# Kernel optimization log

Measured on AMD Instinct MI355X. Metric: run time of the kernel, lower is better.

The kernel has to match this reference:

```python
import jax, jax.numpy as jnp
import numpy as np

N_PAIRS = 64000
N_ATOMS = 16000
N_PAIR_FEATURES = 8
N_HIDDEN = 100


def setup_inputs() -> dict:
    key = jax.random.key(0)
    k1, k2, k3, k4 = jax.random.split(key, 4)
    pair_features = jax.random.normal(k1, (N_PAIRS, N_PAIR_FEATURES), dtype=jnp.float32)
    atom_features = jax.random.normal(k2, (N_ATOMS, N_HIDDEN), dtype=jnp.float32)
    atom_to_pair = jax.random.randint(k3, (N_PAIRS, 2), 0, N_ATOMS, dtype=jnp.int32)
    W = jax.random.normal(k4, (N_PAIR_FEATURES, N_HIDDEN * N_HIDDEN), dtype=jnp.float32) * 0.1
    b = jnp.zeros((N_HIDDEN * N_HIDDEN,), dtype=jnp.float32)
    return {"pair_features": pair_features, "atom_features": atom_features,
            "atom_to_pair": atom_to_pair, "W": W, "b": b}


def reference(pair_features, atom_features, atom_to_pair, W, b):
    n_atoms, n_hidden = atom_features.shape
    # Dense projection: [E, F] @ [F, H*H] -> per-edge HxH matrices
    A = (pair_features @ W + b).reshape(-1, n_hidden, n_hidden)  # [E, H, H]
    # Gather source-atom features (column 1 of atom_to_pair)
    src = atom_features[atom_to_pair[:, 1]]                      # [E, H]
    # Batched matrix-vector multiply per edge
    msg = jnp.einsum('eij,ej->ei', A, src)                       # [E, H]
    # Scatter-reduce messages onto destination atoms (column 0)
    return jax.ops.segment_sum(msg, atom_to_pair[:, 0], num_segments=n_atoms)
```

## Files before the change

kernel.cpp:

```cpp
#include <hip/hip_runtime.h>
#include <hip/hip_bf16.h>

#define N_PAIRS   64000
#define N_ATOMS   16000
#define N_FEAT    8
#define N_HIDDEN  100
#define SW        1024
#define SKL       936
#define MAX_DEG   64

#define SETUP_BLOCKS (112 * 1024 / 256)
#define HIST_BLOCKS  (N_PAIRS / 256)

typedef __attribute__((ext_vector_type(8))) short bf16x8_t;
typedef __attribute__((ext_vector_type(4))) float f32x4_t;

__global__ __launch_bounds__(256) void setup_hist(const float* __restrict__ W,
                                                  const float* __restrict__ b,
                                                  const int* __restrict__ a2p,
                                                  const float* __restrict__ pf,
                                                  __hip_bfloat16* __restrict__ wtb2,
                                                  int* __restrict__ deg,
                                                  unsigned* __restrict__ bucket,
                                                  float* __restrict__ pfb) {
    int bid = blockIdx.x;
    if (bid < SETUP_BLOCKS) {
        int id = bid * 256 + threadIdx.x;
        int i = id >> 10;
        int k = id & 1023;
        float v = 0.f;
        if (i < N_HIDDEN) {
            if (k < 800) {
                int f = k / N_HIDDEN;
                int j = k - f * N_HIDDEN;
                v = W[f * (N_HIDDEN * N_HIDDEN) + i * N_HIDDEN + j];
            } else if (k < 900) {
                int j = k - 800;
                v = b[i * N_HIDDEN + j];
            }
        }
        wtb2[id] = __float2bfloat16(v);
    } else {
        int e = (bid - SETUP_BLOCKS) * 256 + threadIdx.x;
        int dest = a2p[e * 2];
        int src  = a2p[e * 2 + 1];
        int slot = atomicAdd(&deg[dest], 1);
        if (slot < MAX_DEG) {
            bucket[dest * MAX_DEG + slot] = (unsigned)src;
            const float4* ps = (const float4*)(pf + e * N_FEAT);
            float4* pd = (float4*)(pfb + ((size_t)dest * MAX_DEG + slot) * N_FEAT);
            pd[0] = ps[0];
            pd[1] = ps[1];
        }
    }
}

__global__ __launch_bounds__(512) void fused_edge_gemm(const float* __restrict__ af,
                                                       const int* __restrict__ deg,
                                                       const unsigned* __restrict__ bucket,
                                                       const float* __restrict__ pfb,
                                                       const __hip_bfloat16* __restrict__ wtb2,
                                                       float* __restrict__ out) {
    __shared__ __hip_bfloat16 St[16 * SKL];
    int blk  = blockIdx.x;
    int wave = threadIdx.x >> 6;
    int lane = threadIdx.x & 63;
    bool act = (lane < 50);

#pragma unroll
    for (int j = 0; j < 2; ++j) {
        int r = wave * 2 + j;
        int d = __builtin_amdgcn_readfirstlane(blk * 16 + r);
        int n = deg[d];
        if (n > 32) n = 32;

        const unsigned* sb  = bucket + (size_t)d * MAX_DEG;
        const float*    pfd = pfb + (size_t)d * MAX_DEG * N_FEAT;

        float acc[9][2] = {};
        for (int t0 = 0; t0 < n; t0 += 4) {
            float2 a[4];
#pragma unroll
            for (int u = 0; u < 4; ++u) {
                int t = t0 + u;
                int src = (int)sb[t < n ? t : 0];
                if (t < n && act)
                    a[u] = *(const float2*)(af + src * N_HIDDEN + 2 * lane);
                else
                    a[u] = make_float2(0.f, 0.f);
            }
#pragma unroll
            for (int u = 0; u < 4; ++u) {
                int t = t0 + u;
                const float* pe = pfd + t * N_FEAT;
#pragma unroll
                for (int f = 0; f < N_FEAT; ++f) {
                    float p = pe[f];
                    acc[f][0] += p * a[u].x;
                    acc[f][1] += p * a[u].y;
                }
                acc[8][0] += a[u].x;
                acc[8][1] += a[u].y;
            }
        }

        __hip_bfloat16* srow = St + r * SKL;
        if (act) {
#pragma unroll
            for (int f = 0; f < 9; ++f) {
                __hip_bfloat162 h;
                h.x = __float2bfloat16(acc[f][0]);
                h.y = __float2bfloat16(acc[f][1]);
                *(__hip_bfloat162*)(srow + f * N_HIDDEN + 2 * lane) = h;
            }
        } else if (lane < 64) {
            __hip_bfloat162 z;
            z.x = __float2bfloat16(0.f);
            z.y = z.x;
            *(__hip_bfloat162*)(srow + 900 + 2 * (lane - 50)) = z;
        }
    }
    __syncthreads();

    if (wave < 7) {
        int quad = lane >> 4;
        int l15  = lane & 15;
        int m0   = blk * 16;
        const __hip_bfloat16* as = St + l15 * SKL + quad * 8;
        const __hip_bfloat16* bp = wtb2 + (size_t)(wave * 16 + l15) * SW + quad * 8;
        f32x4_t accd = {0.f, 0.f, 0.f, 0.f};
#pragma unroll
        for (int k = 0; k < 29; ++k) {
            bf16x8_t aa = *(const bf16x8_t*)(as + k * 32);
            bf16x8_t bb = *(const bf16x8_t*)(bp + k * 32);
            accd = __builtin_amdgcn_mfma_f32_16x16x32_bf16(aa, bb, accd, 0, 0, 0);
        }
        int c = wave * 16 + l15;
        if (c < N_HIDDEN) {
#pragma unroll
            for (int rr = 0; rr < 4; ++rr)
                out[(size_t)(m0 + quad * 4 + rr) * N_HIDDEN + c] = accd[rr];
        }
    }
}

extern "C" void kernel_launch(void* const* d_in, const int* in_sizes, int n_in,
                              void* d_out, int out_size, void* d_ws, size_t ws_size,
                              hipStream_t stream) {
    const float* pf  = (const float*)d_in[0];
    const float* af  = (const float*)d_in[1];
    const int*   a2p = (const int*)d_in[2];
    const float* W   = (const float*)d_in[3];
    const float* b   = (const float*)d_in[4];
    float* out = (float*)d_out;

    char* ws = (char*)d_ws;
    __hip_bfloat16* wtb2 = (__hip_bfloat16*)ws;
    int* deg             = (int*)(ws + 229376);
    unsigned* bucket     = (unsigned*)(ws + 229376 + 64000);
    float* pfb           = (float*)(ws + 229376 + 64000 + 4096000);

    hipMemsetAsync(deg, 0, N_ATOMS * sizeof(int), stream);
    setup_hist<<<SETUP_BLOCKS + HIST_BLOCKS, 256, 0, stream>>>(W, b, a2p, pf, wtb2, deg, bucket, pfb);
    fused_edge_gemm<<<N_ATOMS / 16, 512, 0, stream>>>(af, deg, bucket, pfb, wtb2, out);
}
```

Before: 105.7 us.

## Convert atom features to bf16 and pack edge index into bucket instead of copying pair features

```diff
diff --git a/kernel.cpp b/kernel.cpp
--- a/kernel.cpp
+++ b/kernel.cpp
@@ -9,6 +9,7 @@
 #define SKL       936
 #define MAX_DEG   64
 
+#define AFB_BLOCKS   1563
 #define SETUP_BLOCKS (112 * 1024 / 256)
 #define HIST_BLOCKS  (N_PAIRS / 256)
 
@@ -18,14 +19,25 @@
 __global__ __launch_bounds__(256) void setup_hist(const float* __restrict__ W,
                                                   const float* __restrict__ b,
                                                   const int* __restrict__ a2p,
-                                                  const float* __restrict__ pf,
+                                                  const float* __restrict__ af,
                                                   __hip_bfloat16* __restrict__ wtb2,
+                                                  unsigned short* __restrict__ afb,
                                                   int* __restrict__ deg,
-                                                  unsigned* __restrict__ bucket,
-                                                  float* __restrict__ pfb) {
+                                                  unsigned* __restrict__ bucket) {
     int bid = blockIdx.x;
-    if (bid < SETUP_BLOCKS) {
+    if (bid < AFB_BLOCKS) {
         int id = bid * 256 + threadIdx.x;
+        if (id < 400000) {
+            float4 v = ((const float4*)af)[id];
+            ushort4 h;
+            h.x = (unsigned short)(__float_as_uint(v.x) >> 16);
+            h.y = (unsigned short)(__float_as_uint(v.y) >> 16);
+            h.z = (unsigned short)(__float_as_uint(v.z) >> 16);
+            h.w = (unsigned short)(__float_as_uint(v.w) >> 16);
+            ((ushort4*)afb)[id] = h;
+        }
+    } else if (bid < AFB_BLOCKS + SETUP_BLOCKS) {
+        int id = (bid - AFB_BLOCKS) * 256 + threadIdx.x;
         int i = id >> 10;
         int k = id & 1023;
         float v = 0.f;
@@ -41,24 +53,19 @@
         }
         wtb2[id] = __float2bfloat16(v);
     } else {
-        int e = (bid - SETUP_BLOCKS) * 256 + threadIdx.x;
+        int e = (bid - AFB_BLOCKS - SETUP_BLOCKS) * 256 + threadIdx.x;
         int dest = a2p[e * 2];
         int src  = a2p[e * 2 + 1];
         int slot = atomicAdd(&deg[dest], 1);
-        if (slot < MAX_DEG) {
-            bucket[dest * MAX_DEG + slot] = (unsigned)src;
-            const float4* ps = (const float4*)(pf + e * N_FEAT);
-            float4* pd = (float4*)(pfb + ((size_t)dest * MAX_DEG + slot) * N_FEAT);
-            pd[0] = ps[0];
-            pd[1] = ps[1];
-        }
+        if (slot < MAX_DEG)
+            bucket[dest * MAX_DEG + slot] = ((unsigned)e << 14) | (unsigned)src;
     }
 }
 
-__global__ __launch_bounds__(512) void fused_edge_gemm(const float* __restrict__ af,
+__global__ __launch_bounds__(512) void fused_edge_gemm(const unsigned short* __restrict__ afb,
+                                                       const float* __restrict__ pf,
                                                        const int* __restrict__ deg,
                                                        const unsigned* __restrict__ bucket,
-                                                       const float* __restrict__ pfb,
                                                        const __hip_bfloat16* __restrict__ wtb2,
                                                        float* __restrict__ out) {
     __shared__ __hip_bfloat16 St[16 * SKL];
@@ -74,25 +81,30 @@
         int n = deg[d];
         if (n > 32) n = 32;
 
-        const unsigned* sb  = bucket + (size_t)d * MAX_DEG;
-        const float*    pfd = pfb + (size_t)d * MAX_DEG * N_FEAT;
+        const unsigned* sb = bucket + (size_t)d * MAX_DEG;
 
         float acc[9][2] = {};
         for (int t0 = 0; t0 < n; t0 += 4) {
+            unsigned pk[4];
+#pragma unroll
+            for (int u = 0; u < 4; ++u)
+                pk[u] = sb[(t0 + u) < n ? (t0 + u) : 0];
             float2 a[4];
 #pragma unroll
             for (int u = 0; u < 4; ++u) {
-                int t = t0 + u;
-                int src = (int)sb[t < n ? t : 0];
-                if (t < n && act)
-                    a[u] = *(const float2*)(af + src * N_HIDDEN + 2 * lane);
-                else
+                int src = (int)(pk[u] & 16383u);
+                if ((t0 + u) < n && act) {
+                    unsigned uu = *(const unsigned*)(afb + src * N_HIDDEN + 2 * lane);
+                    a[u].x = __uint_as_float(uu << 16);
+                    a[u].y = __uint_as_float(uu & 0xffff0000u);
+                } else {
                     a[u] = make_float2(0.f, 0.f);
+                }
             }
 #pragma unroll
             for (int u = 0; u < 4; ++u) {
-                int t = t0 + u;
-                const float* pe = pfd + t * N_FEAT;
+                int e = (int)(pk[u] >> 14);
+                const float* pe = pf + e * N_FEAT;
 #pragma unroll
                 for (int f = 0; f < N_FEAT; ++f) {
                     float p = pe[f];
@@ -113,7 +125,7 @@
                 h.y = __float2bfloat16(acc[f][1]);
                 *(__hip_bfloat162*)(srow + f * N_HIDDEN + 2 * lane) = h;
             }
-        } else if (lane < 64) {
+        } else {
             __hip_bfloat162 z;
             z.x = __float2bfloat16(0.f);
             z.y = z.x;
@@ -158,9 +170,10 @@
     __hip_bfloat16* wtb2 = (__hip_bfloat16*)ws;
     int* deg             = (int*)(ws + 229376);
     unsigned* bucket     = (unsigned*)(ws + 229376 + 64000);
-    float* pfb           = (float*)(ws + 229376 + 64000 + 4096000);
+    unsigned short* afb  = (unsigned short*)(ws + 229376 + 64000 + 4096000);
 
     hipMemsetAsync(deg, 0, N_ATOMS * sizeof(int), stream);
-    setup_hist<<<SETUP_BLOCKS + HIST_BLOCKS, 256, 0, stream>>>(W, b, a2p, pf, wtb2, deg, bucket, pfb);
-    fused_edge_gemm<<<N_ATOMS / 16, 512, 0, stream>>>(af, deg, bucket, pfb, wtb2, out);
+    setup_hist<<<AFB_BLOCKS + SETUP_BLOCKS + HIST_BLOCKS, 256, 0, stream>>>(
+        W, b, a2p, af, wtb2, afb, deg, bucket);
+    fused_edge_gemm<<<N_ATOMS / 16, 512, 0, stream>>>(afb, pf, deg, bucket, wtb2, out);
 }
```

After: 106.9 us. No clear change (+1.2%).

## Pre-stage bf16 source features per destination slot via source-side scatter kernel

Applied to the files above, without the earlier changes.

```diff
diff --git a/kernel.cpp b/kernel.cpp
--- a/kernel.cpp
+++ b/kernel.cpp
@@ -7,7 +7,9 @@
 #define N_HIDDEN  100
 #define SW        1024
 #define SKL       936
-#define MAX_DEG   64
+#define BD        32
+#define BS        24
+#define EST       128
 
 #define SETUP_BLOCKS (112 * 1024 / 256)
 #define HIST_BLOCKS  (N_PAIRS / 256)
@@ -20,9 +22,11 @@
                                                   const int* __restrict__ a2p,
                                                   const float* __restrict__ pf,
                                                   __hip_bfloat16* __restrict__ wtb2,
-                                                  int* __restrict__ deg,
-                                                  unsigned* __restrict__ bucket,
-                                                  float* __restrict__ pfb) {
+                                                  int* __restrict__ deg_d,
+                                                  int* __restrict__ deg_s,
+                                                  unsigned* __restrict__ bucket_dest,
+                                                  unsigned* __restrict__ bsrc,
+                                                  float* __restrict__ pfe) {
     int bid = blockIdx.x;
     if (bid < SETUP_BLOCKS) {
         int id = bid * 256 + threadIdx.x;
@@ -42,23 +46,55 @@
         wtb2[id] = __float2bfloat16(v);
     } else {
         int e = (bid - SETUP_BLOCKS) * 256 + threadIdx.x;
-        int dest = a2p[e * 2];
-        int src  = a2p[e * 2 + 1];
-        int slot = atomicAdd(&deg[dest], 1);
-        if (slot < MAX_DEG) {
-            bucket[dest * MAX_DEG + slot] = (unsigned)src;
+        int d = a2p[e * 2];
+        int s = a2p[e * 2 + 1];
+        int slot_d = atomicAdd(&deg_d[d], 1);
+        if (slot_d < BD)
+            bucket_dest[d * BD + slot_d] = ((unsigned)e << 14) | (unsigned)s;
+        unsigned val = 0xFFFFFFFFu;
+        if (slot_d < 8) {
+            val = (unsigned)(d * 8 + slot_d);
             const float4* ps = (const float4*)(pf + e * N_FEAT);
-            float4* pd = (float4*)(pfb + ((size_t)dest * MAX_DEG + slot) * N_FEAT);
+            float4* pd = (float4*)(pfe + (size_t)(d * 8 + slot_d) * N_FEAT);
             pd[0] = ps[0];
             pd[1] = ps[1];
         }
+        int slot_s = atomicAdd(&deg_s[s], 1);
+        if (slot_s < BS)
+            bsrc[s * BS + slot_s] = val;
+    }
+}
+
+__global__ __launch_bounds__(256) void stage_kernel(const float* __restrict__ af,
+                                                    const int* __restrict__ deg_s,
+                                                    const unsigned* __restrict__ bsrc,
+                                                    unsigned short* __restrict__ eaf) {
+    int wave = threadIdx.x >> 6;
+    int lane = threadIdx.x & 63;
+    int s = __builtin_amdgcn_readfirstlane(blockIdx.x * 4 + wave);
+    int ds = deg_s[s];
+    if (ds > BS) ds = BS;
+    bool act = (lane < 50);
+
+    unsigned u = 0;
+    if (act) {
+        float2 v = *(const float2*)(af + s * N_HIDDEN + 2 * lane);
+        u = (__float_as_uint(v.y) & 0xFFFF0000u) | (__float_as_uint(v.x) >> 16);
+    }
+    const unsigned* sb = bsrc + s * BS;
+    for (int t = 0; t < ds; ++t) {
+        unsigned slot = sb[t];
+        if (slot != 0xFFFFFFFFu && act)
+            *(unsigned*)(eaf + (size_t)slot * EST + 2 * lane) = u;
     }
 }
 
 __global__ __launch_bounds__(512) void fused_edge_gemm(const float* __restrict__ af,
-                                                       const int* __restrict__ deg,
-                                                       const unsigned* __restrict__ bucket,
-                                                       const float* __restrict__ pfb,
+                                                       const float* __restrict__ pf,
+                                                       const int* __restrict__ deg_d,
+                                                       const unsigned* __restrict__ bucket_dest,
+                                                       const float* __restrict__ pfe,
+                                                       const unsigned short* __restrict__ eaf,
                                                        const __hip_bfloat16* __restrict__ wtb2,
                                                        float* __restrict__ out) {
     __shared__ __hip_bfloat16 St[16 * SKL];
@@ -71,28 +107,50 @@
     for (int j = 0; j < 2; ++j) {
         int r = wave * 2 + j;
         int d = __builtin_amdgcn_readfirstlane(blk * 16 + r);
-        int n = deg[d];
-        if (n > 32) n = 32;
-
-        const unsigned* sb  = bucket + (size_t)d * MAX_DEG;
-        const float*    pfd = pfb + (size_t)d * MAX_DEG * N_FEAT;
+        int n = deg_d[d];
+        if (n > BD) n = BD;
+        int ns = n < 8 ? n : 8;
+
+        const unsigned short* ebase = eaf + (size_t)d * 8 * EST;
+        unsigned uu[8];
+#pragma unroll
+        for (int t = 0; t < 8; ++t)
+            uu[t] = (t < ns && act) ? *(const unsigned*)(ebase + t * EST + 2 * lane) : 0u;
+
+        const float* pp = pfe + (size_t)d * 64;
 
         float acc[9][2] = {};
-        for (int t0 = 0; t0 < n; t0 += 4) {
+#pragma unroll
+        for (int t = 0; t < 8; ++t) {
+            float ax = __uint_as_float(uu[t] << 16);
+            float ay = __uint_as_float(uu[t] & 0xFFFF0000u);
+#pragma unroll
+            for (int f = 0; f < N_FEAT; ++f) {
+                float p = pp[t * 8 + f];
+                acc[f][0] += p * ax;
+                acc[f][1] += p * ay;
+            }
+            acc[8][0] += ax;
+            acc[8][1] += ay;
+        }
+        const unsigned* sbd = bucket_dest + (size_t)d * BD;
+        for (int t0 = 8; t0 < n; t0 += 4) {
+            unsigned pk[4];
+#pragma unroll
+            for (int u = 0; u < 4; ++u)
+                pk[u] = sbd[(t0 + u) < n ? (t0 + u) : 0];
             float2 a[4];
 #pragma unroll
             for (int u = 0; u < 4; ++u) {
-                int t = t0 + u;
-                int src = (int)sb[t < n ? t : 0];
-                if (t < n && act)
-                    a[u] = *(const float2*)(af + src * N_HIDDEN + 2 * lane);
-                else
-                    a[u] = make_float2(0.f, 0.f);
+                int src = (int)(pk[u] & 16383u);
+                a[u] = ((t0 + u) < n && act)
+                     ? *(const float2*)(af + src * N_HIDDEN + 2 * lane)
+                     : make_float2(0.f, 0.f);
             }
 #pragma unroll
             for (int u = 0; u < 4; ++u) {
-                int t = t0 + u;
-                const float* pe = pfd + t * N_FEAT;
+                int e = (int)(pk[u] >> 14);
+                const float* pe = pf + e * N_FEAT;
 #pragma unroll
                 for (int f = 0; f < N_FEAT; ++f) {
                     float p = pe[f];
@@ -113,7 +171,7 @@
                 h.y = __float2bfloat16(acc[f][1]);
                 *(__hip_bfloat162*)(srow + f * N_HIDDEN + 2 * lane) = h;
             }
-        } else if (lane < 64) {
+        } else {
             __hip_bfloat162 z;
             z.x = __float2bfloat16(0.f);
             z.y = z.x;
@@ -155,12 +213,18 @@
     float* out = (float*)d_out;
 
     char* ws = (char*)d_ws;
-    __hip_bfloat16* wtb2 = (__hip_bfloat16*)ws;
-    int* deg             = (int*)(ws + 229376);
-    unsigned* bucket     = (unsigned*)(ws + 229376 + 64000);
-    float* pfb           = (float*)(ws + 229376 + 64000 + 4096000);
-
-    hipMemsetAsync(deg, 0, N_ATOMS * sizeof(int), stream);
-    setup_hist<<<SETUP_BLOCKS + HIST_BLOCKS, 256, 0, stream>>>(W, b, a2p, pf, wtb2, deg, bucket, pfb);
-    fused_edge_gemm<<<N_ATOMS / 16, 512, 0, stream>>>(af, deg, bucket, pfb, wtb2, out);
-}
+    __hip_bfloat16* wtb2     = (__hip_bfloat16*)ws;
+    int* deg_d               = (int*)(ws + 229376);
+    int* deg_s               = (int*)(ws + 293376);
+    unsigned* bucket_dest    = (unsigned*)(ws + 357376);
+    unsigned* bsrc           = (unsigned*)(ws + 2405376);
+    float* pfe               = (float*)(ws + 3941376);
+    unsigned short* eaf      = (unsigned short*)(ws + 8037376);
+
+    hipMemsetAsync(ws + 229376, 0, 128000, stream);
+    setup_hist<<<SETUP_BLOCKS + HIST_BLOCKS, 256, 0, stream>>>(
+        W, b, a2p, pf, wtb2, deg_d, deg_s, bucket_dest, bsrc, pfe);
+    stage_kernel<<<N_ATOMS / 4, 256, 0, stream>>>(af, deg_s, bsrc, eaf);
+    fused_edge_gemm<<<N_ATOMS / 16, 512, 0, stream>>>(
+        af, pf, deg_d, bucket_dest, pfe, eaf, wtb2, out);
+}
```

New measurement: 118.5 us. 12.1% more time.
